# Kernel optimization log

Hardware: AMD Instinct MI355X
Metric: run time of the kernel (lower is better)

Reference implementation:

```python
import jax, jax.numpy as jnp
import numpy as np

MUL = 128          # hidden multiplicity for both 0e and 1o
OUT_MUL = 16       # output multiplicity for 0e and 1o
INV_SQRT_MUL = 1.0 / np.sqrt(MUL).astype(np.float32)


def setup_inputs() -> dict:
    key = jax.random.key(0)
    k_x, k1s, k1v, k2s, k2v = jax.random.split(key, 5)
    N = 200000
    # node features: 128 scalars (0e) followed by 128 vectors (1o, 3 components each)
    x = jax.random.normal(k_x, (N, MUL + 3 * MUL), dtype=jnp.float32)
    # e3nn Linear weights are standard normal; path norm 1/sqrt(fan_in) applied in forward
    w1_s = jax.random.normal(k1s, (MUL, 2 * MUL), dtype=jnp.float32)  # 128x0e -> 256x0e (scalars + gates)
    w1_v = jax.random.normal(k1v, (MUL, MUL), dtype=jnp.float32)      # 128x1o -> 128x1o
    w2_s = jax.random.normal(k2s, (MUL, OUT_MUL), dtype=jnp.float32)  # 128x0e -> 16x0e
    w2_v = jax.random.normal(k2v, (MUL, OUT_MUL), dtype=jnp.float32)  # 128x1o -> 16x1o
    return {"x": x, "w1_s": w1_s, "w1_v": w1_v, "w2_s": w2_s, "w2_v": w2_v}


def reference(x, w1_s, w1_v, w2_s, w2_v):
    N = x.shape[0]
    s = x[:, :MUL]                                   # [N, 128] scalars 0e
    v = x[:, MUL:].reshape(N, MUL, 3)                # [N, 128, 3] vectors 1o

    # --- Linear 1: hidden -> 256x0e + 128x1o (block-diagonal per irrep) ---
    h_s = (s @ w1_s) * INV_SQRT_MUL                  # [N, 256]
    h_v = jnp.einsum('nmc,mk->nkc', v, w1_v) * INV_SQRT_MUL  # [N, 128, 3]

    # --- Gate: leading 128 scalars -> silu, trailing 128 scalars gate vectors ---
    act_s = jax.nn.silu(h_s[:, :MUL])                # [N, 128]
    gates = jax.nn.sigmoid(h_s[:, MUL:])             # [N, 128]
    gated_v = h_v * gates[:, :, None]                # [N, 128, 3]

    # --- Linear 2: 128x0e + 128x1o -> 16x0e + 16x1o ---
    out_s = (act_s @ w2_s) * INV_SQRT_MUL            # [N, 16]
    out_v = jnp.einsum('nmc,mk->nkc', gated_v, w2_v) * INV_SQRT_MUL  # [N, 16, 3]

    return jnp.concatenate([out_s, out_v.reshape(N, 3 * OUT_MUL)], axis=1)  # [N, 64]
```

## Files before the change

### kernel.cpp

```cpp
#include <hip/hip_runtime.h>

typedef short bx8 __attribute__((ext_vector_type(8)));
typedef unsigned short ux4 __attribute__((ext_vector_type(4)));
typedef float fx4 __attribute__((ext_vector_type(4)));

#define INV 0.08838834764831843f
#define LP 136
#define TR 16
#define NROWS 200000
#define NT (NROWS / TR)
#define NTHREADS 640
#define NBLOCKS 256

__device__ __forceinline__ unsigned short f2bf(float f) {
  unsigned u = __builtin_bit_cast(unsigned, f);
  u += 0x7FFFu + ((u >> 16) & 1u);
  return (unsigned short)(u >> 16);
}
__device__ __forceinline__ float bf2f(unsigned short h) {
  unsigned u = ((unsigned)h) << 16;
  return __builtin_bit_cast(float, u);
}
__device__ __forceinline__ float sigm(float z) { return 1.0f / (1.0f + __expf(-z)); }

__global__ __launch_bounds__(NTHREADS) void nlr_kernel(
    const float* __restrict__ x, const float* __restrict__ w1_s,
    const float* __restrict__ w1_v, const float* __restrict__ w2_s,
    const float* __restrict__ w2_v, float* __restrict__ out) {
  __shared__ short lds[9 * TR * LP];
  short* X = lds;
  short* ACT = lds + 4 * TR * LP;
  short* GS = lds + 8 * TR * LP;

  const int tid = threadIdx.x;
  const int w = tid >> 6;
  const int lane = tid & 63;
  const int quad = lane >> 4;
  const int c16 = lane & 15;
  const int mrow0 = quad * 8;

  const bool hasS = tid < 512;
  const bool hasV = (tid < 384) || (tid >= 512);
  const int sn = tid >> 5, sch = tid & 31;
  const int vu = (tid < 384) ? (tid + 128) : (tid - 512);
  const int vn = vu >> 5, vch = vu & 31;

  bx8 Wf[4][4];
  if (w < 4) {
#pragma unroll
    for (int jjb = 0; jjb < 4; ++jjb) {
      const int col = (w * 4 + jjb) * 16 + c16;
#pragma unroll
      for (int kb = 0; kb < 4; ++kb) {
        bx8 f;
#pragma unroll
        for (int jj = 0; jj < 8; ++jj)
          f[jj] = (short)f2bf(w1_s[(kb * 32 + mrow0 + jj) * 256 + col]);
        Wf[jjb][kb] = f;
      }
    }
  } else {
    const int half = (w - 4) & 1;
#pragma unroll
    for (int jjb = 0; jjb < 4; ++jjb) {
      const int col = (half * 4 + jjb) * 16 + c16;
#pragma unroll
      for (int kb = 0; kb < 4; ++kb) {
        bx8 f;
#pragma unroll
        for (int jj = 0; jj < 8; ++jj)
          f[jj] = (short)f2bf(w1_v[(kb * 32 + mrow0 + jj) * 128 + col]);
        Wf[jjb][kb] = f;
      }
    }
  }
  bx8 W2f[4];
  {
    const float* w2 = (w == 0) ? w2_s : w2_v;
#pragma unroll
    for (int kb = 0; kb < 4; ++kb) {
      bx8 f;
#pragma unroll
      for (int jj = 0; jj < 8; ++jj)
        f[jj] = (short)f2bf(w2[(kb * 32 + mrow0 + jj) * 16 + c16]);
      W2f[kb] = f;
    }
  }

  fx4 pf_s, pf_a, pf_b, pf_c;

  int tile = blockIdx.x;
  {
    const float* xb = x + (size_t)tile * (TR * 512);
    if (hasS) pf_s = *(const fx4*)(xb + sn * 512 + sch * 4);
    if (hasV) {
      const float* bp = xb + vn * 512 + 128 + vch * 12;
      pf_a = *(const fx4*)bp; pf_b = *(const fx4*)(bp + 4); pf_c = *(const fx4*)(bp + 8);
    }
  }

  while (tile < NT) {
    if (hasS) {
      ux4 p = {f2bf(pf_s[0]), f2bf(pf_s[1]), f2bf(pf_s[2]), f2bf(pf_s[3])};
      *(ux4*)(X + sn * LP + sch * 4) = p;
    }
    if (hasV) {
      ux4 p0 = {f2bf(pf_a[0]), f2bf(pf_a[3]), f2bf(pf_b[2]), f2bf(pf_c[1])};
      ux4 p1 = {f2bf(pf_a[1]), f2bf(pf_b[0]), f2bf(pf_b[3]), f2bf(pf_c[2])};
      ux4 p2 = {f2bf(pf_a[2]), f2bf(pf_b[1]), f2bf(pf_c[0]), f2bf(pf_c[3])};
      *(ux4*)(X + 1 * TR * LP + vn * LP + vch * 4) = p0;
      *(ux4*)(X + 2 * TR * LP + vn * LP + vch * 4) = p1;
      *(ux4*)(X + 3 * TR * LP + vn * LP + vch * 4) = p2;
    }
    const int nxt = tile + NBLOCKS;
    __syncthreads();

    if (nxt < NT) {
      const float* xb = x + (size_t)nxt * (TR * 512);
      if (hasS) pf_s = *(const fx4*)(xb + sn * 512 + sch * 4);
      if (hasV) {
        const float* bp = xb + vn * 512 + 128 + vch * 12;
        pf_a = *(const fx4*)bp; pf_b = *(const fx4*)(bp + 4); pf_c = *(const fx4*)(bp + 8);
      }
    }

    fx4 acc[4];
    {
      const short* src = (w < 4) ? X : (X + (1 + ((w - 4) >> 1)) * TR * LP);
      bx8 B[4];
      const int rbase = c16 * LP + mrow0;
#pragma unroll
      for (int kb = 0; kb < 4; ++kb) B[kb] = *(const bx8*)(src + rbase + kb * 32);
#pragma unroll
      for (int jjb = 0; jjb < 4; ++jjb) {
        fx4 a = {0.f, 0.f, 0.f, 0.f};
#pragma unroll
        for (int kb = 0; kb < 4; ++kb)
          a = __builtin_amdgcn_mfma_f32_16x16x32_bf16(Wf[jjb][kb], B[kb], a, 0, 0, 0);
        acc[jjb] = a;
      }
    }
    if (w == 2 || w == 3) {
#pragma unroll
      for (int jjb = 0; jjb < 4; ++jjb) {
        const int jb = w * 4 + jjb;
        ux4 p;
#pragma unroll
        for (int r = 0; r < 4; ++r) p[r] = f2bf(sigm(acc[jjb][r] * INV));
        *(ux4*)(GS + c16 * LP + (jb - 8) * 16 + quad * 4) = p;
      }
    }
    __syncthreads();

    if (w < 2) {
#pragma unroll
      for (int jjb = 0; jjb < 4; ++jjb) {
        const int jb = w * 4 + jjb;
        ux4 p;
#pragma unroll
        for (int r = 0; r < 4; ++r) {
          const float h = acc[jjb][r] * INV;
          p[r] = f2bf(h * sigm(h));
        }
        *(ux4*)(ACT + c16 * LP + jb * 16 + quad * 4) = p;
      }
    } else if (w >= 4) {
      const int vc = (w - 4) >> 1, half = (w - 4) & 1;
      short* gv = ACT + (1 + vc) * TR * LP;
#pragma unroll
      for (int jjb = 0; jjb < 4; ++jjb) {
        const int jb = half * 4 + jjb;
        const ux4 g = *(const ux4*)(GS + c16 * LP + jb * 16 + quad * 4);
        ux4 p;
#pragma unroll
        for (int r = 0; r < 4; ++r)
          p[r] = f2bf(acc[jjb][r] * INV * bf2f(g[r]));
        *(ux4*)(gv + c16 * LP + jb * 16 + quad * 4) = p;
      }
    }
    __syncthreads();

    if (w < 4) {
      const short* src = ACT + w * TR * LP;
      fx4 a = {0.f, 0.f, 0.f, 0.f};
      const int rbase = c16 * LP + mrow0;
#pragma unroll
      for (int kb = 0; kb < 4; ++kb) {
        const bx8 B = *(const bx8*)(src + rbase + kb * 32);
        a = __builtin_amdgcn_mfma_f32_16x16x32_bf16(W2f[kb], B, a, 0, 0, 0);
      }
      const size_t n = (size_t)tile * TR + c16;
      if (w == 0) {
        fx4 o = {a[0] * INV, a[1] * INV, a[2] * INV, a[3] * INV};
        *(fx4*)(out + n * 64 + quad * 4) = o;
      } else {
        const int c = w - 1;
#pragma unroll
        for (int r = 0; r < 4; ++r)
          out[n * 64 + 16 + 3 * (quad * 4 + r) + c] = a[r] * INV;
      }
    }
    tile = nxt;
  }
}

extern "C" void kernel_launch(void* const* d_in, const int* in_sizes, int n_in,
                              void* d_out, int out_size, void* d_ws, size_t ws_size,
                              hipStream_t stream) {
  const float* x    = (const float*)d_in[0];
  const float* w1_s = (const float*)d_in[1];
  const float* w1_v = (const float*)d_in[2];
  const float* w2_s = (const float*)d_in[3];
  const float* w2_v = (const float*)d_in[4];
  nlr_kernel<<<NBLOCKS, NTHREADS, 0, stream>>>(x, w1_s, w1_v, w2_s, w2_v, (float*)d_out);
}
```

Baseline: 580.2 us.

## Raise occupancy: move W2 fragments to LDS, drop register prefetch, double blocks

Moves the second-layer weight fragments out of per-thread registers into shared memory and removes the register-held software prefetch of the next input tile. Adds a min-blocks hint to launch bounds and doubles the grid to 512 blocks. The aim is to cut VGPR pressure so more blocks fit per CU and latency is hidden by occupancy instead of explicit prefetch. In exchange the input load is no longer overlapped within a block, and the second GEMM now reads its weights from LDS on every tile.

```diff
diff --git a/kernel.cpp b/kernel.cpp
--- a/kernel.cpp
+++ b/kernel.cpp
@@ -10,7 +10,7 @@
 #define NROWS 200000
 #define NT (NROWS / TR)
 #define NTHREADS 640
-#define NBLOCKS 256
+#define NBLOCKS 512
 
 __device__ __forceinline__ unsigned short f2bf(float f) {
   unsigned u = __builtin_bit_cast(unsigned, f);
@@ -23,14 +23,15 @@
 }
 __device__ __forceinline__ float sigm(float z) { return 1.0f / (1.0f + __expf(-z)); }
 
-__global__ __launch_bounds__(NTHREADS) void nlr_kernel(
+__global__ __launch_bounds__(NTHREADS, 5) void nlr_kernel(
     const float* __restrict__ x, const float* __restrict__ w1_s,
     const float* __restrict__ w1_v, const float* __restrict__ w2_s,
     const float* __restrict__ w2_v, float* __restrict__ out) {
-  __shared__ short lds[9 * TR * LP];
+  __shared__ short lds[9 * TR * LP + 4 * 4 * 64 * 8];
   short* X = lds;
   short* ACT = lds + 4 * TR * LP;
   short* GS = lds + 8 * TR * LP;
+  short* W2L = lds + 9 * TR * LP;
 
   const int tid = threadIdx.x;
   const int w = tid >> 6;
@@ -74,8 +75,8 @@
       }
     }
   }
-  bx8 W2f[4];
-  {
+
+  if (w < 4) {
     const float* w2 = (w == 0) ? w2_s : w2_v;
 #pragma unroll
     for (int kb = 0; kb < 4; ++kb) {
@@ -83,46 +84,33 @@
 #pragma unroll
       for (int jj = 0; jj < 8; ++jj)
         f[jj] = (short)f2bf(w2[(kb * 32 + mrow0 + jj) * 16 + c16]);
-      W2f[kb] = f;
+      *(bx8*)(W2L + ((w * 4 + kb) * 64 + lane) * 8) = f;
     }
   }
 
-  fx4 pf_s, pf_a, pf_b, pf_c;
-
   int tile = blockIdx.x;
-  {
-    const float* xb = x + (size_t)tile * (TR * 512);
-    if (hasS) pf_s = *(const fx4*)(xb + sn * 512 + sch * 4);
-    if (hasV) {
-      const float* bp = xb + vn * 512 + 128 + vch * 12;
-      pf_a = *(const fx4*)bp; pf_b = *(const fx4*)(bp + 4); pf_c = *(const fx4*)(bp + 8);
-    }
-  }
-
   while (tile < NT) {
-    if (hasS) {
-      ux4 p = {f2bf(pf_s[0]), f2bf(pf_s[1]), f2bf(pf_s[2]), f2bf(pf_s[3])};
-      *(ux4*)(X + sn * LP + sch * 4) = p;
-    }
-    if (hasV) {
-      ux4 p0 = {f2bf(pf_a[0]), f2bf(pf_a[3]), f2bf(pf_b[2]), f2bf(pf_c[1])};
-      ux4 p1 = {f2bf(pf_a[1]), f2bf(pf_b[0]), f2bf(pf_b[3]), f2bf(pf_c[2])};
-      ux4 p2 = {f2bf(pf_a[2]), f2bf(pf_b[1]), f2bf(pf_c[0]), f2bf(pf_c[3])};
-      *(ux4*)(X + 1 * TR * LP + vn * LP + vch * 4) = p0;
-      *(ux4*)(X + 2 * TR * LP + vn * LP + vch * 4) = p1;
-      *(ux4*)(X + 3 * TR * LP + vn * LP + vch * 4) = p2;
-    }
-    const int nxt = tile + NBLOCKS;
-    __syncthreads();
-
-    if (nxt < NT) {
-      const float* xb = x + (size_t)nxt * (TR * 512);
-      if (hasS) pf_s = *(const fx4*)(xb + sn * 512 + sch * 4);
+    {
+      const float* xb = x + (size_t)tile * (TR * 512);
+      if (hasS) {
+        const fx4 sv = *(const fx4*)(xb + sn * 512 + sch * 4);
+        ux4 p = {f2bf(sv[0]), f2bf(sv[1]), f2bf(sv[2]), f2bf(sv[3])};
+        *(ux4*)(X + sn * LP + sch * 4) = p;
+      }
       if (hasV) {
         const float* bp = xb + vn * 512 + 128 + vch * 12;
-        pf_a = *(const fx4*)bp; pf_b = *(const fx4*)(bp + 4); pf_c = *(const fx4*)(bp + 8);
-      }
-    }
+        const fx4 va = *(const fx4*)bp;
+        const fx4 vb = *(const fx4*)(bp + 4);
+        const fx4 vc = *(const fx4*)(bp + 8);
+        ux4 p0 = {f2bf(va[0]), f2bf(va[3]), f2bf(vb[2]), f2bf(vc[1])};
+        ux4 p1 = {f2bf(va[1]), f2bf(vb[0]), f2bf(vb[3]), f2bf(vc[2])};
+        ux4 p2 = {f2bf(va[2]), f2bf(vb[1]), f2bf(vc[0]), f2bf(vc[3])};
+        *(ux4*)(X + 1 * TR * LP + vn * LP + vch * 4) = p0;
+        *(ux4*)(X + 2 * TR * LP + vn * LP + vch * 4) = p1;
+        *(ux4*)(X + 3 * TR * LP + vn * LP + vch * 4) = p2;
+      }
+    }
+    __syncthreads();
 
     fx4 acc[4];
     {
@@ -182,12 +170,14 @@
 
     if (w < 4) {
       const short* src = ACT + w * TR * LP;
+      const short* wfl = W2L + (w * 4 * 64 + lane) * 8;
       fx4 a = {0.f, 0.f, 0.f, 0.f};
       const int rbase = c16 * LP + mrow0;
 #pragma unroll
       for (int kb = 0; kb < 4; ++kb) {
-        const bx8 B = *(const bx8*)(src + rbase + kb * 32);
-        a = __builtin_amdgcn_mfma_f32_16x16x32_bf16(W2f[kb], B, a, 0, 0, 0);
+        const bx8 Bf = *(const bx8*)(src + rbase + kb * 32);
+        const bx8 Af = *(const bx8*)(wfl + kb * 64 * 8);
+        a = __builtin_amdgcn_mfma_f32_16x16x32_bf16(Af, Bf, a, 0, 0, 0);
       }
       const size_t n = (size_t)tile * TR + c16;
       if (w == 0) {
@@ -200,7 +190,7 @@
           out[n * 64 + 16 + 3 * (quad * 4 + r) + c] = a[r] * INV;
       }
     }
-    tile = nxt;
+    tile += NBLOCKS;
   }
 }
 
```

Result: slower. 756.9 us (+30.5%).

## Triple-buffer x via async global-to-LDS loads and stage output through LDS

Applied to the files above, without the earlier changes.

Input tiles are now copied straight from global memory into a three-slot fp32 LDS ring with global_load_lds, issued two tiles ahead and gated by explicit vmcnt waits. The bf16 conversion and the vector deinterleave move into the MFMA operand loads, replacing the register prefetch and conversion stage. Outputs go to an LDS buffer and are written back by two otherwise idle waves one iteration later as coalesced 16-byte stores, instead of strided scalar stores. This aims to hide load latency and improve store coalescing, at the cost of more LDS, strided LDS reads for the vector operands, and hand-written waitcnt logic that must match the issue pattern.

```diff
diff --git a/kernel.cpp b/kernel.cpp
--- a/kernel.cpp
+++ b/kernel.cpp
@@ -5,12 +5,28 @@
 typedef float fx4 __attribute__((ext_vector_type(4)));
 
 #define INV 0.08838834764831843f
-#define LP 136
 #define TR 16
 #define NROWS 200000
 #define NT (NROWS / TR)
 #define NTHREADS 640
 #define NBLOCKS 256
+#define LP32 540
+#define XBUF (TR * LP32)
+#define LPA 136
+#define LPO 68
+
+#define GL16(gp, lp)                                                   \
+  __builtin_amdgcn_global_load_lds(                                    \
+      (const __attribute__((address_space(1))) unsigned*)(gp),         \
+      (__attribute__((address_space(3))) unsigned*)(lp), 16, 0, 0)
+#define FENCE() asm volatile("" ::: "memory")
+#define WAITL0() asm volatile("s_waitcnt lgkmcnt(0)" ::: "memory")
+#define BARRIER()                  \
+  do {                             \
+    WAITL0();                      \
+    __builtin_amdgcn_s_barrier();  \
+    FENCE();                       \
+  } while (0)
 
 __device__ __forceinline__ unsigned short f2bf(float f) {
   unsigned u = __builtin_bit_cast(unsigned, f);
@@ -27,10 +43,10 @@
     const float* __restrict__ x, const float* __restrict__ w1_s,
     const float* __restrict__ w1_v, const float* __restrict__ w2_s,
     const float* __restrict__ w2_v, float* __restrict__ out) {
-  __shared__ short lds[9 * TR * LP];
-  short* X = lds;
-  short* ACT = lds + 4 * TR * LP;
-  short* GS = lds + 8 * TR * LP;
+  __shared__ __align__(16) float XF[3 * XBUF];
+  __shared__ __align__(16) short ACTL[4 * TR * LPA];
+  __shared__ __align__(16) short GSL[TR * LPA];
+  __shared__ __align__(16) float OUTB[TR * LPO];
 
   const int tid = threadIdx.x;
   const int w = tid >> 6;
@@ -39,11 +55,20 @@
   const int c16 = lane & 15;
   const int mrow0 = quad * 8;
 
-  const bool hasS = tid < 512;
-  const bool hasV = (tid < 384) || (tid >= 512);
-  const int sn = tid >> 5, sch = tid & 31;
-  const int vu = (tid < 384) ? (tid + 128) : (tid - 512);
-  const int vn = vu >> 5, vch = vu & 31;
+  auto issue = [&](int t, int buf) {
+    const float* gb = x + (size_t)t * (TR * 512) + 2 * w * 512 + lane * 4;
+    float* lb = XF + buf * XBUF + 2 * w * LP32;
+#pragma unroll
+    for (int j = 0; j < 4; ++j) {
+      const int row = j >> 1, half = j & 1;
+      GL16(gb + row * 512 + half * 256, lb + row * LP32 + half * 256);
+    }
+  };
+
+  if (w < 8) {
+    if ((int)blockIdx.x < NT) issue(blockIdx.x, 0);
+    if ((int)blockIdx.x + NBLOCKS < NT) issue(blockIdx.x + NBLOCKS, 1);
+  }
 
   bx8 Wf[4][4];
   if (w < 4) {
@@ -75,7 +100,7 @@
     }
   }
   bx8 W2f[4];
-  {
+  if (w < 4) {
     const float* w2 = (w == 0) ? w2_s : w2_v;
 #pragma unroll
     for (int kb = 0; kb < 4; ++kb) {
@@ -87,50 +112,63 @@
     }
   }
 
-  fx4 pf_s, pf_a, pf_b, pf_c;
-
   int tile = blockIdx.x;
-  {
-    const float* xb = x + (size_t)tile * (TR * 512);
-    if (hasS) pf_s = *(const fx4*)(xb + sn * 512 + sch * 4);
-    if (hasV) {
-      const float* bp = xb + vn * 512 + 128 + vch * 12;
-      pf_a = *(const fx4*)bp; pf_b = *(const fx4*)(bp + 4); pf_c = *(const fx4*)(bp + 8);
-    }
-  }
-
+  int p = 0;
   while (tile < NT) {
-    if (hasS) {
-      ux4 p = {f2bf(pf_s[0]), f2bf(pf_s[1]), f2bf(pf_s[2]), f2bf(pf_s[3])};
-      *(ux4*)(X + sn * LP + sch * 4) = p;
-    }
-    if (hasV) {
-      ux4 p0 = {f2bf(pf_a[0]), f2bf(pf_a[3]), f2bf(pf_b[2]), f2bf(pf_c[1])};
-      ux4 p1 = {f2bf(pf_a[1]), f2bf(pf_b[0]), f2bf(pf_b[3]), f2bf(pf_c[2])};
-      ux4 p2 = {f2bf(pf_a[2]), f2bf(pf_b[1]), f2bf(pf_c[0]), f2bf(pf_c[3])};
-      *(ux4*)(X + 1 * TR * LP + vn * LP + vch * 4) = p0;
-      *(ux4*)(X + 2 * TR * LP + vn * LP + vch * 4) = p1;
-      *(ux4*)(X + 3 * TR * LP + vn * LP + vch * 4) = p2;
-    }
-    const int nxt = tile + NBLOCKS;
-    __syncthreads();
-
-    if (nxt < NT) {
-      const float* xb = x + (size_t)nxt * (TR * 512);
-      if (hasS) pf_s = *(const fx4*)(xb + sn * 512 + sch * 4);
-      if (hasV) {
-        const float* bp = xb + vn * 512 + 128 + vch * 12;
-        pf_a = *(const fx4*)bp; pf_b = *(const fx4*)(bp + 4); pf_c = *(const fx4*)(bp + 8);
+    const bool h2 = tile + 2 * NBLOCKS < NT;
+    const bool h1 = tile + NBLOCKS < NT;
+    if (h2 && w < 8) {
+      int p2 = p + 2; if (p2 >= 3) p2 -= 3;
+      issue(tile + 2 * NBLOCKS, p2);
+    }
+    if (w < 8) {
+      if (h2)      asm volatile("s_waitcnt vmcnt(8)" ::: "memory");
+      else if (h1) asm volatile("s_waitcnt vmcnt(4)" ::: "memory");
+      else         asm volatile("s_waitcnt vmcnt(0)" ::: "memory");
+    }
+    __builtin_amdgcn_sched_barrier(0);
+    BARRIER();
+
+    if (w >= 8 && tile != (int)blockIdx.x) {
+      const int tprev = tile - NBLOCKS;
+      float* og = out + (size_t)tprev * (TR * 64);
+      const int rbase = (w - 8) * 8;
+#pragma unroll
+      for (int j = 0; j < 2; ++j) {
+        const int row = rbase + j * 4 + quad;
+        const fx4 v = *(const fx4*)(OUTB + row * LPO + c16 * 4);
+        *(fx4*)(og + row * 64 + c16 * 4) = v;
       }
     }
 
     fx4 acc[4];
     {
-      const short* src = (w < 4) ? X : (X + (1 + ((w - 4) >> 1)) * TR * LP);
       bx8 B[4];
-      const int rbase = c16 * LP + mrow0;
-#pragma unroll
-      for (int kb = 0; kb < 4; ++kb) B[kb] = *(const bx8*)(src + rbase + kb * 32);
+      if (w < 4) {
+        const float* xr = XF + p * XBUF + c16 * LP32;
+#pragma unroll
+        for (int kb = 0; kb < 4; ++kb) {
+          const fx4 u0 = *(const fx4*)(xr + kb * 32 + mrow0);
+          const fx4 u1 = *(const fx4*)(xr + kb * 32 + mrow0 + 4);
+          bx8 f;
+          f[0] = (short)f2bf(u0[0]); f[1] = (short)f2bf(u0[1]);
+          f[2] = (short)f2bf(u0[2]); f[3] = (short)f2bf(u0[3]);
+          f[4] = (short)f2bf(u1[0]); f[5] = (short)f2bf(u1[1]);
+          f[6] = (short)f2bf(u1[2]); f[7] = (short)f2bf(u1[3]);
+          B[kb] = f;
+        }
+      } else {
+        const int c = (w - 4) >> 1;
+        const float* xr = XF + p * XBUF + c16 * LP32 + 128 + c;
+#pragma unroll
+        for (int kb = 0; kb < 4; ++kb) {
+          const float* q = xr + 3 * (kb * 32 + mrow0);
+          bx8 f;
+#pragma unroll
+          for (int jj = 0; jj < 8; ++jj) f[jj] = (short)f2bf(q[3 * jj]);
+          B[kb] = f;
+        }
+      }
 #pragma unroll
       for (int jjb = 0; jjb < 4; ++jjb) {
         fx4 a = {0.f, 0.f, 0.f, 0.f};
@@ -144,63 +182,76 @@
 #pragma unroll
       for (int jjb = 0; jjb < 4; ++jjb) {
         const int jb = w * 4 + jjb;
-        ux4 p;
-#pragma unroll
-        for (int r = 0; r < 4; ++r) p[r] = f2bf(sigm(acc[jjb][r] * INV));
-        *(ux4*)(GS + c16 * LP + (jb - 8) * 16 + quad * 4) = p;
-      }
-    }
-    __syncthreads();
+        ux4 pk;
+#pragma unroll
+        for (int r = 0; r < 4; ++r) pk[r] = f2bf(sigm(acc[jjb][r] * INV));
+        *(ux4*)(GSL + c16 * LPA + (jb - 8) * 16 + quad * 4) = pk;
+      }
+    }
+    BARRIER();
 
     if (w < 2) {
 #pragma unroll
       for (int jjb = 0; jjb < 4; ++jjb) {
         const int jb = w * 4 + jjb;
-        ux4 p;
+        ux4 pk;
 #pragma unroll
         for (int r = 0; r < 4; ++r) {
           const float h = acc[jjb][r] * INV;
-          p[r] = f2bf(h * sigm(h));
+          pk[r] = f2bf(h * sigm(h));
         }
-        *(ux4*)(ACT + c16 * LP + jb * 16 + quad * 4) = p;
+        *(ux4*)(ACTL + c16 * LPA + jb * 16 + quad * 4) = pk;
       }
     } else if (w >= 4) {
       const int vc = (w - 4) >> 1, half = (w - 4) & 1;
-      short* gv = ACT + (1 + vc) * TR * LP;
+      short* gv = ACTL + (1 + vc) * TR * LPA;
 #pragma unroll
       for (int jjb = 0; jjb < 4; ++jjb) {
         const int jb = half * 4 + jjb;
-        const ux4 g = *(const ux4*)(GS + c16 * LP + jb * 16 + quad * 4);
-        ux4 p;
+        const ux4 g = *(const ux4*)(GSL + c16 * LPA + jb * 16 + quad * 4);
+        ux4 pk;
 #pragma unroll
         for (int r = 0; r < 4; ++r)
-          p[r] = f2bf(acc[jjb][r] * INV * bf2f(g[r]));
-        *(ux4*)(gv + c16 * LP + jb * 16 + quad * 4) = p;
-      }
-    }
-    __syncthreads();
+          pk[r] = f2bf(acc[jjb][r] * INV * bf2f(g[r]));
+        *(ux4*)(gv + c16 * LPA + jb * 16 + quad * 4) = pk;
+      }
+    }
+    BARRIER();
 
     if (w < 4) {
-      const short* src = ACT + w * TR * LP;
+      const short* src = ACTL + w * TR * LPA;
       fx4 a = {0.f, 0.f, 0.f, 0.f};
-      const int rbase = c16 * LP + mrow0;
+      const int rb = c16 * LPA + mrow0;
 #pragma unroll
       for (int kb = 0; kb < 4; ++kb) {
-        const bx8 B = *(const bx8*)(src + rbase + kb * 32);
-        a = __builtin_amdgcn_mfma_f32_16x16x32_bf16(W2f[kb], B, a, 0, 0, 0);
-      }
-      const size_t n = (size_t)tile * TR + c16;
+        const bx8 Bf = *(const bx8*)(src + rb + kb * 32);
+        a = __builtin_amdgcn_mfma_f32_16x16x32_bf16(W2f[kb], Bf, a, 0, 0, 0);
+      }
       if (w == 0) {
         fx4 o = {a[0] * INV, a[1] * INV, a[2] * INV, a[3] * INV};
-        *(fx4*)(out + n * 64 + quad * 4) = o;
+        *(fx4*)(OUTB + c16 * LPO + quad * 4) = o;
       } else {
         const int c = w - 1;
 #pragma unroll
         for (int r = 0; r < 4; ++r)
-          out[n * 64 + 16 + 3 * (quad * 4 + r) + c] = a[r] * INV;
-      }
-    }
-    tile = nxt;
+          OUTB[c16 * LPO + 16 + 3 * (quad * 4 + r) + c] = a[r] * INV;
+      }
+    }
+    tile += NBLOCKS;
+    p = (p + 1 == 3) ? 0 : p + 1;
+  }
+
+  BARRIER();
+  if (w >= 8) {
+    const int tlast = tile - NBLOCKS;
+    float* og = out + (size_t)tlast * (TR * 64);
+    const int rbase = (w - 8) * 8;
+#pragma unroll
+    for (int j = 0; j < 2; ++j) {
+      const int row = rbase + j * 4 + quad;
+      const fx4 v = *(const fx4*)(OUTB + row * LPO + c16 * 4);
+      *(fx4*)(og + row * 64 + c16 * 4) = v;
+    }
   }
 }
 
```

Measured after the change: 607.6 us. 4.7% more time.
